# Kernel tuning notes

Hardware: AMD Instinct MI355X
Metric: run time of the kernel (lower is better)

## Reference

```python
import jax, jax.numpy as jnp
import numpy as np

B, T, D = 8, 2048, 1024
EPS = 1e-5

def _layernorm(x, g, b):
    mu = jnp.mean(x, axis=-1, keepdims=True)
    var = jnp.mean(jnp.square(x - mu), axis=-1, keepdims=True)
    return (x - mu) * jax.lax.rsqrt(var + EPS) * g + b

def setup_inputs() -> dict:
    key = jax.random.key(0)
    ks = jax.random.split(key, 8)
    scale = 1.0 / np.sqrt(D)
    text_inputs = jax.random.normal(ks[0], (B, T, D), dtype=jnp.float32)
    sit_mask = jax.random.randint(ks[1], (B, T), 0, 2).astype(jnp.float32)
    Wq = jax.random.normal(ks[2], (D, D), dtype=jnp.float32) * scale
    Wk = jax.random.normal(ks[3], (D, D), dtype=jnp.float32) * scale
    Wv = jax.random.normal(ks[4], (D, D), dtype=jnp.float32) * scale
    Wf1 = jax.random.normal(ks[5], (D, D), dtype=jnp.float32) * scale
    bf1 = jnp.zeros((D,), dtype=jnp.float32)
    Wf2 = jax.random.normal(ks[6], (D, D), dtype=jnp.float32) * scale
    bf2 = jnp.zeros((D,), dtype=jnp.float32)
    ln1_g = jnp.ones((D,), dtype=jnp.float32)
    ln1_b = jnp.zeros((D,), dtype=jnp.float32)
    ln2_g = jnp.ones((D,), dtype=jnp.float32)
    ln2_b = jnp.zeros((D,), dtype=jnp.float32)
    return dict(text_inputs=text_inputs, sit_mask=sit_mask, Wq=Wq, Wk=Wk, Wv=Wv,
                ln1_g=ln1_g, ln1_b=ln1_b, Wf1=Wf1, bf1=bf1, Wf2=Wf2, bf2=bf2,
                ln2_g=ln2_g, ln2_b=ln2_b)

def reference(text_inputs, sit_mask, Wq, Wk, Wv, ln1_g, ln1_b, Wf1, bf1, Wf2, bf2, ln2_g, ln2_b):
    x = text_inputs  # [B,T,D]
    d = x.shape[-1]
    # torch Linear: y = x @ W.T
    q = jnp.einsum('btd,ed->bte', x, Wq)
    k = jnp.einsum('btd,ed->bte', x, Wk)
    v = jnp.einsum('btd,ed->bte', x, Wv)
    # scaled scores with causal (strictly-upper = -inf) mask
    scores = jnp.einsum('btd,bsd->bts', q, k) / jnp.sqrt(jnp.asarray(d, x.dtype))
    causal = jnp.tril(jnp.ones((x.shape[1], x.shape[1]), dtype=bool))  # keep diag + past
    scores = jnp.where(causal[None], scores, -jnp.inf)
    attn = jax.nn.softmax(scores, axis=-1)
    # per-batch SIT padding mask applied AFTER softmax (rows may not sum to 1)
    pad_keep = (sit_mask[:, :, None] * sit_mask[:, None, :]) != 0  # [B,T,T]
    attn = jnp.where(pad_keep, attn, 0.0)
    att_out = jnp.einsum('bts,bsd->btd', attn, v)
    # residual + LN, FFN (Linear-ReLU-Linear), residual + LN
    h = _layernorm(att_out + x, ln1_g, ln1_b)
    ff = jnp.einsum('btd,ed->bte', jax.nn.relu(jnp.einsum('btd,ed->bte', h, Wf1) + bf1), Wf2) + bf2
    out = _layernorm(ff + h, ln2_g, ln2_b)
    return out
```

## Files before the change

### kernel.cpp

```cpp
#include <hip/hip_runtime.h>

typedef unsigned short ushort_t;
typedef __attribute__((ext_vector_type(8))) __bf16 bf16x8;
typedef __attribute__((ext_vector_type(4))) float f32x4;
typedef __attribute__((ext_vector_type(4))) int i32x4;
typedef __attribute__((ext_vector_type(4))) unsigned short u16x4;
typedef __attribute__((ext_vector_type(8))) unsigned short u16x8;

__device__ __forceinline__ float bf2f(ushort_t u) {
  union { unsigned u32; float f; } c; c.u32 = ((unsigned)u) << 16; return c.f;
}
__device__ __forceinline__ ushort_t f2bf(float f) {
  union { float f; unsigned u32; } c; c.f = f;
  unsigned u = c.u32;
  u += 0x7fffu + ((u >> 16) & 1u);
  return (ushort_t)(u >> 16);
}

__device__ __forceinline__ void gload_lds16(const void* g, void* l) {
  __builtin_amdgcn_global_load_lds(
      (const __attribute__((address_space(1))) void*)g,
      (__attribute__((address_space(3))) void*)l,
      16, 0, 0);
}

__device__ __forceinline__ void stage_half(const char* gbase, long row0, int ldbytes,
                                           int kbyte, char* lds_half, int tid)
{
  const int rl = tid >> 3;
  const int cs = ((tid & 7) ^ (rl & 7)) << 4;
  const char* g0 = gbase + (row0 + rl) * (long)ldbytes + kbyte + cs;
  char* l0 = lds_half + ((tid >> 6) << 10);
  gload_lds16(g0, l0);
  gload_lds16(g0 + (long)ldbytes * 64, l0 + 8192);
}

#define BAR() __builtin_amdgcn_s_barrier()
#define VMW6() asm volatile("s_waitcnt vmcnt(6)" ::: "memory")
#define VMW8() asm volatile("s_waitcnt vmcnt(8)" ::: "memory")
#define PR1() __builtin_amdgcn_s_setprio(1)
#define PR0() __builtin_amdgcn_s_setprio(0)

#define RD_A4(dst, base, rb) \
  _Pragma("unroll") for (int m_ = 0; m_ < 4; ++m_) { \
    const char* p_ = (base) + ((rb) + m_ * 16 + fr) * 128; \
    dst[m_][0] = *(const bf16x8*)(p_ + ch0); \
    dst[m_][1] = *(const bf16x8*)(p_ + ch1); }
#define RD_B2(dst, base, cb) \
  _Pragma("unroll") for (int n_ = 0; n_ < 2; ++n_) { \
    const char* p_ = (base) + ((cb) + n_ * 16 + fr) * 128; \
    dst[n_][0] = *(const bf16x8*)(p_ + ch0); \
    dst[n_][1] = *(const bf16x8*)(p_ + ch1); }

#define G_MM(ib, jb, Aa, Bb) \
  _Pragma("unroll") for (int m_ = 0; m_ < 4; ++m_) \
  _Pragma("unroll") for (int n_ = 0; n_ < 2; ++n_) \
  _Pragma("unroll") for (int s_ = 0; s_ < 2; ++s_) \
    acc[(ib) + m_][(jb) + n_] = __builtin_amdgcn_mfma_f32_16x16x32_bf16( \
        Aa[m_][s_], Bb[n_][s_], acc[(ib) + m_][(jb) + n_], 0, 0, 0);
#define SAE_(t, hh) stage_half(gA, m0 + (hh) * 128, ldab, (t) << 7, AE + (hh) * 16384, tid)
#define SAO_(t, hh) stage_half(gA, m0 + (hh) * 128, ldab, (t) << 7, AO + (hh) * 16384, tid)
#define SBE_(t, hh) stage_half(gB, n0 + (hh) * 128, ldbb, (t) << 7, BE + (hh) * 16384, tid)
#define SBO_(t, hh) stage_half(gB, n0 + (hh) * 128, ldbb, (t) << 7, BO + (hh) * 16384, tid)

template<int EPI, int MAPQ, bool ROUTE>
__global__ __launch_bounds__(512, 1) void gemm256(
    const ushort_t* __restrict__ A, int lda,
    const ushort_t* __restrict__ B, int ldb,
    ushort_t* __restrict__ C0, ushort_t* __restrict__ C1, ushort_t* __restrict__ C2,
    int ldc, const float* __restrict__ bias, float scale, int K)
{
  __shared__ __attribute__((aligned(16))) ushort_t lds[65536];

  int bx, by;
  if (MAPQ == 1) {
    const int flat = blockIdx.y * 4 + blockIdx.x;
    by = ((flat >> 5) << 3) | (flat & 7);
    bx = (flat >> 3) & 3;
  } else if (MAPQ == 2) {
    const int l = blockIdx.x;
    const int c = l & 7, u = l >> 3;
    const int q12 = u / 12;
    by = (q12 << 3) | c;
    bx = u - q12 * 12;
  } else { bx = blockIdx.x; by = blockIdx.y; }

  const int NT = K >> 6, NIT = NT >> 1, NTm1 = NT - 1;

  const int tid = threadIdx.x, lane = tid & 63;
  const int fr = lane & 15, g = lane >> 4, lm = lane & 7;
  const int wv = tid >> 6, wr = wv >> 2, wc = wv & 3;
  const int wrb = wr << 7, wcb = wc << 6;
  const long m0 = (long)by << 8, n0 = (long)bx << 8;

  const char* gA = (const char*)A;
  const char* gB = (const char*)B;
  const int ldab = lda << 1, ldbb = ldb << 1;

  const int ch0 = (g ^ lm) << 4;
  const int ch1 = ((4 | g) ^ lm) << 4;

  char* AE = (char*)lds;
  char* AO = AE + 32768;
  char* BE = AE + 65536;
  char* BO = AE + 98304;

  f32x4 acc[8][4] = {};
  bf16x8 aF[4][2], aG[4][2], bL[2][2], bL2[2][2], bH[2][2];

  SAE_(0, 0); SAE_(0, 1); SBE_(0, 0); SBE_(0, 1);
  SAO_(1, 0); SAO_(1, 1); SBO_(1, 0); SBO_(1, 1);
  VMW8(); BAR();
  RD_A4(aF, AE, wrb); RD_B2(bL, BE, wcb);

  for (int i = 0; i < NIT; ++i) {
    const int t2 = (2 * i + 2 < NTm1) ? 2 * i + 2 : NTm1;
    const int t3 = (2 * i + 3 < NTm1) ? 2 * i + 3 : NTm1;

    PR1(); G_MM(0, 0, aF, bL); PR0();
    RD_B2(bH, BE, wcb + 32);
    BAR();
    PR1(); G_MM(0, 2, aF, bH); PR0();
    RD_A4(aG, AE, wrb + 64);
    BAR();
    PR1(); G_MM(4, 2, aG, bH); PR0();
    BAR();
    PR1(); G_MM(4, 0, aG, bL); PR0();
    SAE_(t2, 0); SAE_(t2, 1); SBE_(t2, 0); SBE_(t2, 1);
    VMW8(); BAR();
    RD_A4(aF, AO, wrb); RD_B2(bL2, BO, wcb);
    PR1(); G_MM(0, 0, aF, bL2); PR0();
    RD_B2(bH, BO, wcb + 32);
    BAR();
    PR1(); G_MM(0, 2, aF, bH); PR0();
    RD_A4(aG, AO, wrb + 64);
    BAR();
    PR1(); G_MM(4, 2, aG, bH); PR0();
    BAR();
    PR1(); G_MM(4, 0, aG, bL2); PR0();
    SAO_(t3, 0); SAO_(t3, 1); SBO_(t3, 0); SBO_(t3, 1);
    VMW8(); BAR();
    RD_A4(aF, AE, wrb); RD_B2(bL, BE, wcb);
  }

  ushort_t* Cd = C0;
  long nc0 = (long)bx << 8;
  if constexpr (ROUTE) {
    const int which = bx >> 2;
    Cd = (which == 0) ? C0 : (which == 1) ? C1 : C2;
    nc0 = (long)(bx & 3) << 8;
  }

  const int cm = g << 2, cn = fr;
#pragma unroll
  for (int i2 = 0; i2 < 8; ++i2)
#pragma unroll
    for (int j2 = 0; j2 < 4; ++j2) {
      const long gm = m0 + wrb + i2 * 16 + cm;
      const long gn = nc0 + wcb + j2 * 16 + cn;
      float bv = 0.f;
      if constexpr (EPI >= 1) bv = bias[gn];
#pragma unroll
      for (int r = 0; r < 4; ++r) {
        float v = acc[i2][j2][r] * scale + bv;
        if constexpr (EPI == 2) v = fmaxf(v, 0.f);
        Cd[(gm + r) * ldc + gn] = f2bf(v);
      }
    }
}

#define A_MM(jb, Aa, Bb) \
  _Pragma("unroll") for (int m_ = 0; m_ < 4; ++m_) \
  _Pragma("unroll") for (int n_ = 0; n_ < 2; ++n_) \
  _Pragma("unroll") for (int s_ = 0; s_ < 2; ++s_) \
    acc[m_][(jb) + n_] = __builtin_amdgcn_mfma_f32_16x16x32_bf16( \
        Aa[m_][s_], Bb[n_][s_], acc[m_][(jb) + n_], 0, 0, 0);
#define SAA_(t, hh, dst) stage_half(gA, m0 + (hh) * 128, ldab, (t) << 7, (dst) + (hh) * 16384, tid)
#define SBA_(t, dst) stage_half(gB, n0, ldbb, (t) << 7, (dst), tid)

template<int EPI, int MAP, bool CKLIM>
__global__ __launch_bounds__(512, 1) void gemmA(
    const ushort_t* __restrict__ A, int lda, long bsA,
    const ushort_t* __restrict__ B, int ldb, long bsB,
    ushort_t* __restrict__ C, int ldc, long bsC,
    const float* __restrict__ bias, float scale, int K)
{
  __shared__ __attribute__((aligned(16))) ushort_t lds[73728];

  int bx, by, bz;
  if (MAP == 1) {
    const int bid = blockIdx.x;
    bz = bid & 7; const int r = bid >> 3;
    by = 0; while ((by + 1) * (by + 2) <= r) ++by;
    bx = r - by * (by + 1);
  } else if (MAP == 2) {
    const int bid = blockIdx.x;
    bz = bid & 7; const int u = bid >> 3;
    by = 7 - (u >> 3); bx = u & 7;
  } else { bx = blockIdx.x; by = blockIdx.y; bz = blockIdx.z; }

  const int NT = CKLIM ? ((by + 1) << 2) : (K >> 6);
  const int NIT = NT >> 1, NTm1 = NT - 1;

  const int tid = threadIdx.x, lane = tid & 63;
  const int fr = lane & 15, g = lane >> 4, lm = lane & 7;
  const int wv = tid >> 6, wr4 = wv >> 1, wc2 = wv & 1;
  const int wrb = wr4 << 6, wcb = wc2 << 6;
  const long m0 = (long)by << 8, n0 = (long)bx << 7;

  const char* gA = (const char*)(A + bz * bsA);
  const char* gB = (const char*)(B + bz * bsB);
  const int ldab = lda << 1, ldbb = ldb << 1;

  const int ch0 = (g ^ lm) << 4;
  const int ch1 = ((4 | g) ^ lm) << 4;

  char* pEA = (char*)lds;          char* pEB = pEA + 32768;
  char* pOA = (char*)lds + 49152;  char* pOB = pOA + 32768;
  char* pSA = (char*)lds + 98304;  char* pSB = pSA + 32768;

  f32x4 acc[4][4] = {};
  bf16x8 aE[4][2], aO[4][2], bLE[2][2], bLO[2][2], bH[2][2];

  SAA_(0, 0, pEA); SAA_(0, 1, pEA); SBA_(0, pEB);
  SAA_(1, 0, pOA); SAA_(1, 1, pOA); SBA_(1, pOB);
  VMW6(); BAR();
  RD_A4(aE, pEA, wrb); RD_B2(bLE, pEB, wcb);

  for (int i = 0; i < NIT; ++i) {
    const int t2 = (2 * i + 2 < NTm1) ? 2 * i + 2 : NTm1;
    const int t3 = (2 * i + 3 < NTm1) ? 2 * i + 3 : NTm1;

    PR1(); A_MM(0, aE, bLE); PR0();
    RD_B2(bH, pEB, wcb + 32);
    SAA_(t2, 0, pSA); SAA_(t2, 1, pSA);
    BAR();
    PR1(); A_MM(2, aE, bH); PR0();
    SBA_(t2, pSB);
    VMW6(); BAR();
    RD_A4(aO, pOA, wrb); RD_B2(bLO, pOB, wcb);
    PR1(); A_MM(0, aO, bLO); PR0();
    RD_B2(bH, pOB, wcb + 32);
    SAA_(t3, 0, pEA); SAA_(t3, 1, pEA);
    BAR();
    PR1(); A_MM(2, aO, bH); PR0();
    SBA_(t3, pEB);
    VMW6(); BAR();
    RD_A4(aE, pSA, wrb); RD_B2(bLE, pSB, wcb);
    char* tA = pEA; pEA = pSA; pSA = pOA; pOA = tA;
    char* tB = pEB; pEB = pSB; pSB = pOB; pOB = tB;
  }

  ushort_t* Cb = C + bz * bsC;
  const int cm = g << 2, cn = fr;
#pragma unroll
  for (int i2 = 0; i2 < 4; ++i2)
#pragma unroll
    for (int j2 = 0; j2 < 4; ++j2) {
      const long gm = m0 + wrb + i2 * 16 + cm;
      const long gn = n0 + wcb + j2 * 16 + cn;
      float bv = 0.f;
      if constexpr (EPI >= 1) bv = bias[gn];
#pragma unroll
      for (int r = 0; r < 4; ++r) {
        float v = acc[i2][j2][r] * scale + bv;
        if constexpr (EPI == 2) v = fmaxf(v, 0.f);
        Cb[(gm + r) * ldc + gn] = f2bf(v);
      }
    }
}

__global__ __launch_bounds__(256) void transpose_bf16(
    const ushort_t* __restrict__ V, int ldv, long bsV,
    ushort_t* __restrict__ Vt, int ldt, long bsT)
{
  __shared__ __attribute__((aligned(16))) ushort_t tile[64][72];
  const int bz = blockIdx.z;
  const ushort_t* Vb = V + bz * bsV;
  ushort_t* Tb = Vt + bz * bsT;
  const long s0 = (long)blockIdx.y << 6;
  const long d0 = (long)blockIdx.x << 6;
  const int tid = threadIdx.x;
  const int r = tid >> 3, c = tid & 7;
#pragma unroll
  for (int hh = 0; hh < 2; ++hh) {
    const int rr = r + hh * 32;
    i32x4 v = *(const i32x4*)(Vb + (s0 + rr) * ldv + d0 + c * 8);
    *(i32x4*)&tile[rr][c * 8] = v;
  }
  __syncthreads();
#pragma unroll
  for (int hh = 0; hh < 2; ++hh) {
    const int dr = r + hh * 32;
    union { ushort_t u[8]; i32x4 v; } t;
#pragma unroll
    for (int j = 0; j < 8; ++j) t.u[j] = tile[c * 8 + j][dr];
    *(i32x4*)(Tb + (d0 + dr) * ldt + s0 + c * 8) = t.v;
  }
}

__global__ __launch_bounds__(256) void softmax_sit(ushort_t* __restrict__ S,
                                                   const float* __restrict__ sit)
{
  __shared__ float red[4];
  const long row = blockIdx.x;
  const int b = (int)(row >> 11);
  const int t = (int)(row & 2047);
  const int n = t + 1;
  const int rup = ((t >> 8) + 1) << 8;
  ushort_t* Srow = S + (row << 11);
  const int tid = threadIdx.x;
  const int i0 = tid << 3;
  const bool act = i0 < rup;

  u16x8 raw = {};
  if (act) raw = *(const u16x8*)(Srow + i0);
  float v[8];
#pragma unroll
  for (int j = 0; j < 8; ++j) v[j] = bf2f(raw[j]);

  float mloc = -3.0e38f;
#pragma unroll
  for (int j = 0; j < 8; ++j) if (i0 + j < n) mloc = fmaxf(mloc, v[j]);
#pragma unroll
  for (int o = 32; o > 0; o >>= 1) mloc = fmaxf(mloc, __shfl_down(mloc, o, 64));
  if ((tid & 63) == 0) red[tid >> 6] = mloc;
  __syncthreads();
  const float m = fmaxf(fmaxf(red[0], red[1]), fmaxf(red[2], red[3]));
  __syncthreads();

  float e[8];
  float sloc = 0.f;
#pragma unroll
  for (int j = 0; j < 8; ++j) {
    e[j] = (i0 + j < n) ? __expf(v[j] - m) : 0.f;
    sloc += e[j];
  }
#pragma unroll
  for (int o = 32; o > 0; o >>= 1) sloc += __shfl_down(sloc, o, 64);
  if ((tid & 63) == 0) red[tid >> 6] = sloc;
  __syncthreads();
  const float l = red[0] + red[1] + red[2] + red[3];

  float inv = 1.f / l;
  if (sit[row] == 0.f) inv = 0.f;
  if (act) {
    const float* sitb = sit + ((long)b << 11) + i0;
    u16x8 out;
#pragma unroll
    for (int j = 0; j < 8; ++j) {
      const float p = (i0 + j < n && sitb[j] != 0.f) ? e[j] * inv : 0.f;
      out[j] = f2bf(p);
    }
    *(u16x8*)(Srow + i0) = out;
  }
}

template<bool RES_F32, bool OUT_F32>
__global__ __launch_bounds__(256) void resid_ln(
    const ushort_t* __restrict__ xin, const void* __restrict__ resv,
    const float* __restrict__ g, const float* __restrict__ be, void* __restrict__ outv)
{
  __shared__ float red[4];
  const long base = (long)blockIdx.x << 10;
  const int tid = threadIdx.x;
  const int i0 = tid << 2;

  const u16x4 xa = *(const u16x4*)(xin + base + i0);
  float v[4];
  if constexpr (RES_F32) {
    const float4 rv = *(const float4*)((const float*)resv + base + i0);
    v[0] = bf2f(xa.x) + rv.x; v[1] = bf2f(xa.y) + rv.y;
    v[2] = bf2f(xa.z) + rv.z; v[3] = bf2f(xa.w) + rv.w;
  } else {
    const u16x4 rb = *(const u16x4*)((const ushort_t*)resv + base + i0);
    v[0] = bf2f(xa.x) + bf2f(rb.x); v[1] = bf2f(xa.y) + bf2f(rb.y);
    v[2] = bf2f(xa.z) + bf2f(rb.z); v[3] = bf2f(xa.w) + bf2f(rb.w);
  }
  float s = v[0] + v[1] + v[2] + v[3];
#pragma unroll
  for (int o = 32; o > 0; o >>= 1) s += __shfl_down(s, o, 64);
  if ((tid & 63) == 0) red[tid >> 6] = s;
  __syncthreads();
  const float mu = (red[0] + red[1] + red[2] + red[3]) * (1.f / 1024.f);
  __syncthreads();
  float s2 = 0.f;
#pragma unroll
  for (int j = 0; j < 4; ++j) { const float d = v[j] - mu; s2 += d * d; }
#pragma unroll
  for (int o = 32; o > 0; o >>= 1) s2 += __shfl_down(s2, o, 64);
  if ((tid & 63) == 0) red[tid >> 6] = s2;
  __syncthreads();
  const float rstd = rsqrtf((red[0] + red[1] + red[2] + red[3]) * (1.f / 1024.f) + 1e-5f);

  const float4 gv = *(const float4*)(g + i0);
  const float4 bv = *(const float4*)(be + i0);
  const float o0 = (v[0] - mu) * rstd * gv.x + bv.x;
  const float o1 = (v[1] - mu) * rstd * gv.y + bv.y;
  const float o2 = (v[2] - mu) * rstd * gv.z + bv.z;
  const float o3 = (v[3] - mu) * rstd * gv.w + bv.w;
  if constexpr (OUT_F32) {
    float4 ov; ov.x = o0; ov.y = o1; ov.z = o2; ov.w = o3;
    *(float4*)((float*)outv + base + i0) = ov;
  } else {
    u16x4 ob = { f2bf(o0), f2bf(o1), f2bf(o2), f2bf(o3) };
    *(u16x4*)((ushort_t*)outv + base + i0) = ob;
  }
}

__global__ __launch_bounds__(256) void cast_f32_bf16(const float* __restrict__ src,
                                                     ushort_t* __restrict__ dst, int n4)
{
  const int i = blockIdx.x * 256 + threadIdx.x;
  if (i >= n4) return;
  const float4 v = *(const float4*)(src + ((long)i << 2));
  u16x4 o = { f2bf(v.x), f2bf(v.y), f2bf(v.z), f2bf(v.w) };
  *(u16x4*)(dst + ((long)i << 2)) = o;
}

__global__ __launch_bounds__(256) void cast_w5(
    const float* __restrict__ s0, const float* __restrict__ s1,
    const float* __restrict__ s2, const float* __restrict__ s3,
    const float* __restrict__ s4, ushort_t* __restrict__ dst)
{
  const int w = blockIdx.y;
  const float* src = (w == 0) ? s0 : (w == 1) ? s1 : (w == 2) ? s2 : (w == 3) ? s3 : s4;
  const long off = (long)w << 20;
  const int i = blockIdx.x * 256 + threadIdx.x;
  const float4 v = *(const float4*)(src + ((long)i << 2));
  u16x4 o = { f2bf(v.x), f2bf(v.y), f2bf(v.z), f2bf(v.w) };
  *(u16x4*)(dst + off + ((long)i << 2)) = o;
}

extern "C" void kernel_launch(void* const* d_in, const int* in_sizes, int n_in,
                              void* d_out, int out_size, void* d_ws, size_t ws_size,
                              hipStream_t stream) {
  const int T = 2048, D = 1024;
  const long TD = (long)T * D;
  const long ND = 8 * TD;
  const float* x    = (const float*)d_in[0];
  const float* sit  = (const float*)d_in[1];
  const float* Wq   = (const float*)d_in[2];
  const float* Wk   = (const float*)d_in[3];
  const float* Wv   = (const float*)d_in[4];
  const float* ln1g = (const float*)d_in[5];
  const float* ln1b = (const float*)d_in[6];
  const float* Wf1  = (const float*)d_in[7];
  const float* bf1  = (const float*)d_in[8];
  const float* Wf2  = (const float*)d_in[9];
  const float* bf2  = (const float*)d_in[10];
  const float* ln2g = (const float*)d_in[11];
  const float* ln2b = (const float*)d_in[12];

  ushort_t* W16 = (ushort_t*)d_ws;
  ushort_t* xb  = W16;
  ushort_t* vb  = W16 + ND;
  ushort_t* S   = W16;
  ushort_t* hb  = W16;
  ushort_t* ff1 = W16 + ND;
  ushort_t* vt  = W16 + 2 * ND;
  ushort_t* ff2 = vt;
  ushort_t* wq  = W16 + 3 * ND;
  ushort_t* wf1 = wq + 3L * D * D;
  ushort_t* wf2 = wf1 + (long)D * D;
  ushort_t* qb = (ushort_t*)d_out;
  ushort_t* kb = qb + ND;
  ushort_t* attb = (ushort_t*)d_out;

  cast_f32_bf16<<<16384, 256, 0, stream>>>(x, xb, (int)(ND / 4));
  cast_w5<<<dim3(1024, 5), 256, 0, stream>>>(Wq, Wk, Wv, Wf1, Wf2, wq);

  gemm256<0, 2, true><<<dim3(768), 512, 0, stream>>>(
      xb, 1024, wq, 1024, qb, kb, vb, 1024, nullptr, 1.f, 1024);

  transpose_bf16<<<dim3(16, 32, 8), 256, 0, stream>>>(vb, 1024, TD, vt, 2048, TD);

  gemmA<0, 1, false><<<dim3(576), 512, 0, stream>>>(
      qb, 1024, TD, kb, 1024, TD, S, 2048, (long)T * T, nullptr, 0.03125f, 1024);

  softmax_sit<<<16384, 256, 0, stream>>>(S, sit);

  gemmA<0, 2, true><<<dim3(512), 512, 0, stream>>>(
      S, 2048, (long)T * T, vt, 2048, TD, attb, 1024, TD, nullptr, 1.f, 2048);

  resid_ln<true, false><<<16384, 256, 0, stream>>>(attb, x, ln1g, ln1b, hb);

  gemm256<2, 1, false><<<dim3(4, 64), 512, 0, stream>>>(
      hb, 1024, wf1, 1024, ff1, ff1, ff1, 1024, bf1, 1.f, 1024);
  gemm256<1, 1, false><<<dim3(4, 64), 512, 0, stream>>>(
      ff1, 1024, wf2, 1024, ff2, ff2, ff2, 1024, bf2, 1.f, 1024);

  resid_ln<false, true><<<16384, 256, 0, stream>>>(ff2, hb, ln2g, ln2b, (float*)d_out);
}
```

Baseline: 394.0 us.

## Trim GEMM barriers, issue prefetch earlier, pair softmax rows per block

In both GEMM main loops, several block barriers are removed. An explicit lgkmcnt(0) wait now precedes the remaining barrier, and global-to-LDS prefetch loads for the next tile are issued one MMA phase earlier, so fewer wavefront stalls and more overlap are expected. The softmax kernel now handles two rows per block, pairing causal row t with its mirror row, so short and long rows share a block and the grid is halved. The risk is LDS races: buffers may be overwritten while other waves still read them if the removed barriers were needed.

After: 392.6 us. Within noise of the previous version (-0.3%).

```diff
diff --git a/kernel.cpp b/kernel.cpp
--- a/kernel.cpp
+++ b/kernel.cpp
@@ -38,6 +38,7 @@
 #define BAR() __builtin_amdgcn_s_barrier()
 #define VMW6() asm volatile("s_waitcnt vmcnt(6)" ::: "memory")
 #define VMW8() asm volatile("s_waitcnt vmcnt(8)" ::: "memory")
+#define LGKM0() asm volatile("s_waitcnt lgkmcnt(0)" ::: "memory")
 #define PR1() __builtin_amdgcn_s_setprio(1)
 #define PR0() __builtin_amdgcn_s_setprio(0)
 
@@ -119,26 +120,22 @@
 
     PR1(); G_MM(0, 0, aF, bL); PR0();
     RD_B2(bH, BE, wcb + 32);
-    BAR();
     PR1(); G_MM(0, 2, aF, bH); PR0();
     RD_A4(aG, AE, wrb + 64);
-    BAR();
+    LGKM0(); BAR();
     PR1(); G_MM(4, 2, aG, bH); PR0();
-    BAR();
+    SAE_(t2, 0); SAE_(t2, 1); SBE_(t2, 0); SBE_(t2, 1);
     PR1(); G_MM(4, 0, aG, bL); PR0();
-    SAE_(t2, 0); SAE_(t2, 1); SBE_(t2, 0); SBE_(t2, 1);
     VMW8(); BAR();
     RD_A4(aF, AO, wrb); RD_B2(bL2, BO, wcb);
     PR1(); G_MM(0, 0, aF, bL2); PR0();
     RD_B2(bH, BO, wcb + 32);
-    BAR();
     PR1(); G_MM(0, 2, aF, bH); PR0();
     RD_A4(aG, AO, wrb + 64);
-    BAR();
+    LGKM0(); BAR();
     PR1(); G_MM(4, 2, aG, bH); PR0();
-    BAR();
+    SAO_(t3, 0); SAO_(t3, 1); SBO_(t3, 0); SBO_(t3, 1);
     PR1(); G_MM(4, 0, aG, bL2); PR0();
-    SAO_(t3, 0); SAO_(t3, 1); SBO_(t3, 0); SBO_(t3, 1);
     VMW8(); BAR();
     RD_A4(aF, AE, wrb); RD_B2(bL, BE, wcb);
   }
@@ -233,19 +230,15 @@
 
     PR1(); A_MM(0, aE, bLE); PR0();
     RD_B2(bH, pEB, wcb + 32);
-    SAA_(t2, 0, pSA); SAA_(t2, 1, pSA);
-    BAR();
+    SAA_(t2, 0, pSA); SAA_(t2, 1, pSA); SBA_(t2, pSB);
     PR1(); A_MM(2, aE, bH); PR0();
-    SBA_(t2, pSB);
-    VMW6(); BAR();
+    LGKM0(); VMW6(); BAR();
     RD_A4(aO, pOA, wrb); RD_B2(bLO, pOB, wcb);
     PR1(); A_MM(0, aO, bLO); PR0();
     RD_B2(bH, pOB, wcb + 32);
-    SAA_(t3, 0, pEA); SAA_(t3, 1, pEA);
-    BAR();
+    SAA_(t3, 0, pEA); SAA_(t3, 1, pEA); SBA_(t3, pEB);
     PR1(); A_MM(2, aO, bH); PR0();
-    SBA_(t3, pEB);
-    VMW6(); BAR();
+    LGKM0(); VMW6(); BAR();
     RD_A4(aE, pSA, wrb); RD_B2(bLE, pSB, wcb);
     char* tA = pEA; pEA = pSA; pSA = pOA; pOA = tA;
     char* tB = pEB; pEB = pSB; pSB = pOB; pOB = tB;
@@ -299,60 +292,82 @@
   }
 }
 
-__global__ __launch_bounds__(256) void softmax_sit(ushort_t* __restrict__ S,
-                                                   const float* __restrict__ sit)
-{
-  __shared__ float red[4];
-  const long row = blockIdx.x;
-  const int b = (int)(row >> 11);
-  const int t = (int)(row & 2047);
-  const int n = t + 1;
-  const int rup = ((t >> 8) + 1) << 8;
-  ushort_t* Srow = S + (row << 11);
+__global__ __launch_bounds__(256) void softmax_sit2(ushort_t* __restrict__ S,
+                                                    const float* __restrict__ sit)
+{
+  __shared__ float redA[4], redB[4];
+  const int bid = blockIdx.x;
+  const long rowA = bid, rowB = 16383 - bid;
+  const int bA = (int)(rowA >> 11), tA = (int)(rowA & 2047);
+  const int bB = (int)(rowB >> 11), tB = (int)(rowB & 2047);
+  const int nA = tA + 1, nB = tB + 1;
+  const int rupA = ((tA >> 8) + 1) << 8, rupB = ((tB >> 8) + 1) << 8;
+  ushort_t* SrA = S + (rowA << 11);
+  ushort_t* SrB = S + (rowB << 11);
   const int tid = threadIdx.x;
   const int i0 = tid << 3;
-  const bool act = i0 < rup;
-
-  u16x8 raw = {};
-  if (act) raw = *(const u16x8*)(Srow + i0);
-  float v[8];
-#pragma unroll
-  for (int j = 0; j < 8; ++j) v[j] = bf2f(raw[j]);
-
-  float mloc = -3.0e38f;
-#pragma unroll
-  for (int j = 0; j < 8; ++j) if (i0 + j < n) mloc = fmaxf(mloc, v[j]);
-#pragma unroll
-  for (int o = 32; o > 0; o >>= 1) mloc = fmaxf(mloc, __shfl_down(mloc, o, 64));
-  if ((tid & 63) == 0) red[tid >> 6] = mloc;
-  __syncthreads();
-  const float m = fmaxf(fmaxf(red[0], red[1]), fmaxf(red[2], red[3]));
-  __syncthreads();
-
-  float e[8];
-  float sloc = 0.f;
+  const bool actA = i0 < rupA, actB = i0 < rupB;
+
+  u16x8 rawA = {}, rawB = {};
+  if (actA) rawA = *(const u16x8*)(SrA + i0);
+  if (actB) rawB = *(const u16x8*)(SrB + i0);
+  float vA[8], vB[8];
+#pragma unroll
+  for (int j = 0; j < 8; ++j) { vA[j] = bf2f(rawA[j]); vB[j] = bf2f(rawB[j]); }
+
+  float mA = -3.0e38f, mB = -3.0e38f;
 #pragma unroll
   for (int j = 0; j < 8; ++j) {
-    e[j] = (i0 + j < n) ? __expf(v[j] - m) : 0.f;
-    sloc += e[j];
-  }
-#pragma unroll
-  for (int o = 32; o > 0; o >>= 1) sloc += __shfl_down(sloc, o, 64);
-  if ((tid & 63) == 0) red[tid >> 6] = sloc;
-  __syncthreads();
-  const float l = red[0] + red[1] + red[2] + red[3];
-
-  float inv = 1.f / l;
-  if (sit[row] == 0.f) inv = 0.f;
-  if (act) {
-    const float* sitb = sit + ((long)b << 11) + i0;
+    if (i0 + j < nA) mA = fmaxf(mA, vA[j]);
+    if (i0 + j < nB) mB = fmaxf(mB, vB[j]);
+  }
+#pragma unroll
+  for (int o = 32; o > 0; o >>= 1) {
+    mA = fmaxf(mA, __shfl_down(mA, o, 64));
+    mB = fmaxf(mB, __shfl_down(mB, o, 64));
+  }
+  if ((tid & 63) == 0) { redA[tid >> 6] = mA; redB[tid >> 6] = mB; }
+  __syncthreads();
+  const float mxA = fmaxf(fmaxf(redA[0], redA[1]), fmaxf(redA[2], redA[3]));
+  const float mxB = fmaxf(fmaxf(redB[0], redB[1]), fmaxf(redB[2], redB[3]));
+  __syncthreads();
+
+  float eA[8], eB[8];
+  float sA = 0.f, sB = 0.f;
+#pragma unroll
+  for (int j = 0; j < 8; ++j) {
+    eA[j] = (i0 + j < nA) ? __expf(vA[j] - mxA) : 0.f;
+    eB[j] = (i0 + j < nB) ? __expf(vB[j] - mxB) : 0.f;
+    sA += eA[j]; sB += eB[j];
+  }
+#pragma unroll
+  for (int o = 32; o > 0; o >>= 1) {
+    sA += __shfl_down(sA, o, 64);
+    sB += __shfl_down(sB, o, 64);
+  }
+  if ((tid & 63) == 0) { redA[tid >> 6] = sA; redB[tid >> 6] = sB; }
+  __syncthreads();
+  const float lA = redA[0] + redA[1] + redA[2] + redA[3];
+  const float lB = redB[0] + redB[1] + redB[2] + redB[3];
+
+  float invA = 1.f / lA, invB = 1.f / lB;
+  if (sit[rowA] == 0.f) invA = 0.f;
+  if (sit[rowB] == 0.f) invB = 0.f;
+  if (actA) {
+    const float* sb = sit + ((long)bA << 11) + i0;
     u16x8 out;
 #pragma unroll
-    for (int j = 0; j < 8; ++j) {
-      const float p = (i0 + j < n && sitb[j] != 0.f) ? e[j] * inv : 0.f;
-      out[j] = f2bf(p);
-    }
-    *(u16x8*)(Srow + i0) = out;
+    for (int j = 0; j < 8; ++j)
+      out[j] = f2bf((i0 + j < nA && sb[j] != 0.f) ? eA[j] * invA : 0.f);
+    *(u16x8*)(SrA + i0) = out;
+  }
+  if (actB) {
+    const float* sb = sit + ((long)bB << 11) + i0;
+    u16x8 out;
+#pragma unroll
+    for (int j = 0; j < 8; ++j)
+      out[j] = f2bf((i0 + j < nB && sb[j] != 0.f) ? eB[j] * invB : 0.f);
+    *(u16x8*)(SrB + i0) = out;
   }
 }
 
@@ -478,7 +493,7 @@
   gemmA<0, 1, false><<<dim3(576), 512, 0, stream>>>(
       qb, 1024, TD, kb, 1024, TD, S, 2048, (long)T * T, nullptr, 0.03125f, 1024);
 
-  softmax_sit<<<16384, 256, 0, stream>>>(S, sit);
+  softmax_sit2<<<8192, 256, 0, stream>>>(S, sit);
 
   gemmA<0, 2, true><<<dim3(512), 512, 0, stream>>>(
       S, 2048, (long)T * T, vt, 2048, TD, attb, 1024, TD, nullptr, 1.f, 2048);
```
